# Kernel optimization log

Hardware: AMD Instinct MI355X
Metric: run time of the kernel (lower is better)

The kernel has to match this reference:

```python
import jax, jax.numpy as jnp
import numpy as np

B, C, H, W = 16, 256, 64, 64
K = 1024

def setup_inputs() -> dict:
    key = jax.random.key(0)
    k1, k2 = jax.random.split(key)
    x = jax.random.normal(k1, (B, C, H, W), dtype=jnp.float32)
    codebook = jax.random.normal(k2, (K, C), dtype=jnp.float32)
    return {"x": x, "codebook": codebook}


def reference(x, codebook):
    b, c, h, w = x.shape
    # (B, C, H, W) -> (B*H*W, C)
    xf = jnp.transpose(x, (0, 2, 3, 1)).reshape(-1, c)
    # Squared euclidean distances to codebook (argmin is the same as for cdist).
    x2 = jnp.sum(xf * xf, axis=-1, keepdims=True)          # (N, 1)
    c2 = jnp.sum(codebook * codebook, axis=-1)               # (K,)
    dist = x2 - 2.0 * jnp.einsum('nc,kc->nk', xf, codebook) + c2  # (N, K)
    idx = jnp.argmin(dist, axis=-1)                          # (N,)
    quant = codebook[idx]                                     # (N, C)
    commitment_loss = jnp.mean((jax.lax.stop_gradient(quant) - xf) ** 2)
    codebook_loss = jnp.mean((quant - jax.lax.stop_gradient(xf)) ** 2)
    # Straight-through estimator
    quant_out = xf + jax.lax.stop_gradient(quant - xf)
    quant_out = jnp.transpose(quant_out.reshape(b, h, w, c), (0, 3, 1, 2))
    indices = idx.reshape(b, h, w)
    return quant_out, codebook_loss, commitment_loss, indices
```

## Files before the change

kernel.cpp:

```cpp
#include <hip/hip_runtime.h>

constexpr int Bn = 16, Cd = 256, Hn = 64, Wn = 64, Kc = 1024;
constexpr int QUANT_ELEMS = Bn * Hn * Wn * Cd;
constexpr int LOSS_OFF = QUANT_ELEMS;
constexpr int IDX_OFF = QUANT_ELEMS + 2;

typedef _Float16 half8 __attribute__((ext_vector_type(8)));
typedef float f32x4 __attribute__((ext_vector_type(4)));

constexpr size_t WS_CBFH = 0;
constexpr size_t WS_CBFL = 512 * 1024;
constexpr size_t WS_C2   = 1024 * 1024;

constexpr float THR = 1e-4f;

__global__ __launch_bounds__(256) void prep(const float* __restrict__ cb,
                                            _Float16* __restrict__ cbFh,
                                            _Float16* __restrict__ cbFl,
                                            float* __restrict__ c2,
                                            float* __restrict__ out) {
    __shared__ float cbs[16][257];
    const int tid = threadIdx.x;
    const int k0 = blockIdx.x * 16;
    {
        const int c4 = (tid & 63) * 4;
        const int r0 = tid >> 6;
        #pragma unroll
        for (int it = 0; it < 4; ++it) {
            const int r = r0 + it * 4;
            const float4 v = *(const float4*)&cb[(size_t)(k0 + r) * Cd + c4];
            cbs[r][c4] = v.x; cbs[r][c4 + 1] = v.y; cbs[r][c4 + 2] = v.z; cbs[r][c4 + 3] = v.w;
        }
    }
    __syncthreads();
    {
        const int i = tid >> 4, part = tid & 15;
        float s = 0.f;
        #pragma unroll
        for (int c = part * 16; c < part * 16 + 16; ++c) { const float v = cbs[i][c]; s += v * v; }
        s += __shfl_xor(s, 1);
        s += __shfl_xor(s, 2);
        s += __shfl_xor(s, 4);
        s += __shfl_xor(s, 8);
        if (part == 0) c2[k0 + i] = s;
    }
    for (int t = tid; t < 512; t += 256) {
        const int kblk = t >> 6;
        const int l = t & 63;
        const int code_l = l & 15;
        const int cbase = kblk * 32 + (l >> 4) * 8;
        half8 hv, lv;
        #pragma unroll
        for (int j = 0; j < 8; ++j) {
            const float v = cbs[code_l][cbase + j];
            const _Float16 hh = (_Float16)v;
            hv[j] = hh;
            lv[j] = (_Float16)(v - (float)hh);
        }
        const size_t e = (size_t)(blockIdx.x * 8 + kblk) * 64 + l;
        *(half8*)(cbFh + e * 8) = hv;
        *(half8*)(cbFl + e * 8) = lv;
    }
    if (blockIdx.x == 0 && tid == 0) {
        out[LOSS_OFF] = 0.f; out[LOSS_OFF + 1] = 0.f;
    }
}

__global__ __launch_bounds__(512, 4) void vq_main(const float* __restrict__ x,
                                                  const _Float16* __restrict__ cbFh,
                                                  const _Float16* __restrict__ cbFl,
                                                  const float* __restrict__ c2,
                                                  const float* __restrict__ cb,
                                                  float* __restrict__ out) {
    __shared__ half8 Axh[2048];
    __shared__ half8 Axl[2048];
    __shared__ float q1ds[8][32];
    __shared__ int   q1is[8][32];
    __shared__ float q2ds[8][32];
    __shared__ int   q2is[8][32];
    __shared__ int   idx_s[64];
    __shared__ float red[8];
    __shared__ int   flg[64];
    __shared__ int   nflag;

    const int tid = threadIdx.x;
    const int lane = tid & 63;
    const int wv = tid >> 6;
    const int mth = wv & 1;
    const int ntq = wv >> 1;
    const int bh = blockIdx.x;
    const int b = bh >> 6, h = bh & 63;

    if (tid == 0) nflag = 0;

    {
        const int m = tid & 15;
        const int q = (tid >> 4) & 3;
        const int mtg = (tid >> 6) & 3;
        const int kh = tid >> 8;
        const int w = mtg * 16 + m;
        const float* xb = x + ((size_t)b * Cd * Hn + h) * Wn + w;
        #pragma unroll
        for (int kk = 0; kk < 4; ++kk) {
            const int kblk = kh * 4 + kk;
            half8 hv, lv;
            #pragma unroll
            for (int j = 0; j < 8; ++j) {
                const int c = kblk * 32 + q * 8 + j;
                const float v = xb[(size_t)c * (Hn * Wn)];
                const _Float16 hh = (_Float16)v;
                hv[j] = hh;
                lv[j] = (_Float16)(v - (float)hh);
            }
            const int e = (kblk * 4 + mtg) * 64 + (q * 16 + m);
            Axh[e] = hv;
            Axl[e] = lv;
        }
    }
    __syncthreads();

    float q1d[8], q2d[8];
    int   q1i[8], q2i[8];
    #pragma unroll
    for (int i = 0; i < 8; ++i) { q1d[i] = 3.4e38f; q2d[i] = 3.4e38f; q1i[i] = 0; q2i[i] = 0; }

    half8 nbh[2], nbl[2];
    #pragma unroll
    for (int nt = 0; nt < 2; ++nt) {
        const int ntile = ntq * 16 + nt;
        const size_t be = ((size_t)(ntile * 8) * 64 + lane) * 8;
        nbh[nt] = *(const half8*)(cbFh + be);
        nbl[nt] = *(const half8*)(cbFl + be);
    }

    #pragma unroll 1
    for (int grp = 0; grp < 8; ++grp) {
        f32x4 acc[2][2];
        acc[0][0] = (f32x4){0.f, 0.f, 0.f, 0.f};
        acc[0][1] = (f32x4){0.f, 0.f, 0.f, 0.f};
        acc[1][0] = (f32x4){0.f, 0.f, 0.f, 0.f};
        acc[1][1] = (f32x4){0.f, 0.f, 0.f, 0.f};

        #pragma unroll 2
        for (int kblk = 0; kblk < 8; ++kblk) {
            const half8 cbh0 = nbh[0], cbh1 = nbh[1];
            const half8 cbl0 = nbl[0], cbl1 = nbl[1];
            {
                const int nk = (kblk + 1) & 7;
                const int ng = (grp + ((kblk + 1) >> 3)) & 7;
                #pragma unroll
                for (int nt = 0; nt < 2; ++nt) {
                    const int ntile = ntq * 16 + ng * 2 + nt;
                    const size_t be = ((size_t)(ntile * 8 + nk) * 64 + lane) * 8;
                    nbh[nt] = *(const half8*)(cbFh + be);
                    nbl[nt] = *(const half8*)(cbFl + be);
                }
            }
            half8 ahf[2], alf[2];
            #pragma unroll
            for (int ml = 0; ml < 2; ++ml) {
                const int e = (kblk * 4 + mth * 2 + ml) * 64 + lane;
                ahf[ml] = Axh[e];
                alf[ml] = Axl[e];
            }
            #pragma unroll
            for (int ml = 0; ml < 2; ++ml) {
                acc[ml][0] = __builtin_amdgcn_mfma_f32_16x16x32_f16(ahf[ml], cbh0, acc[ml][0], 0, 0, 0);
                acc[ml][1] = __builtin_amdgcn_mfma_f32_16x16x32_f16(ahf[ml], cbh1, acc[ml][1], 0, 0, 0);
            }
            #pragma unroll
            for (int ml = 0; ml < 2; ++ml) {
                acc[ml][0] = __builtin_amdgcn_mfma_f32_16x16x32_f16(ahf[ml], cbl0, acc[ml][0], 0, 0, 0);
                acc[ml][1] = __builtin_amdgcn_mfma_f32_16x16x32_f16(ahf[ml], cbl1, acc[ml][1], 0, 0, 0);
            }
            #pragma unroll
            for (int ml = 0; ml < 2; ++ml) {
                acc[ml][0] = __builtin_amdgcn_mfma_f32_16x16x32_f16(alf[ml], cbh0, acc[ml][0], 0, 0, 0);
                acc[ml][1] = __builtin_amdgcn_mfma_f32_16x16x32_f16(alf[ml], cbh1, acc[ml][1], 0, 0, 0);
            }
        }

        #pragma unroll
        for (int nt = 0; nt < 2; ++nt) {
            const int code = (ntq * 16 + grp * 2 + nt) * 16 + (lane & 15);
            const float c2v = c2[code];
            #pragma unroll
            for (int ml = 0; ml < 2; ++ml) {
                #pragma unroll
                for (int reg = 0; reg < 4; ++reg) {
                    const float d = fmaf(-2.f, acc[ml][nt][reg], c2v);
                    const int qi = ml * 4 + reg;
                    const bool b1 = d < q1d[qi];
                    const bool b2 = d < q2d[qi];
                    q2d[qi] = b1 ? q1d[qi] : (b2 ? d : q2d[qi]);
                    q2i[qi] = b1 ? q1i[qi] : (b2 ? code : q2i[qi]);
                    q1d[qi] = b1 ? d : q1d[qi];
                    q1i[qi] = b1 ? code : q1i[qi];
                }
            }
        }
    }

    #pragma unroll
    for (int off = 1; off < 16; off <<= 1) {
        #pragma unroll
        for (int qi = 0; qi < 8; ++qi) {
            const float od1 = __shfl_xor(q1d[qi], off);
            const int   oi1 = __shfl_xor(q1i[qi], off);
            const float od2 = __shfl_xor(q2d[qi], off);
            const int   oi2 = __shfl_xor(q2i[qi], off);
            const bool ob = od1 < q1d[qi];
            const float ld = ob ? q1d[qi] : od1;
            const int   li = ob ? q1i[qi] : oi1;
            const bool o2 = od2 < q2d[qi];
            const float md = o2 ? od2 : q2d[qi];
            const int   mi = o2 ? oi2 : q2i[qi];
            const bool lb = ld < md;
            q2d[qi] = lb ? ld : md;
            q2i[qi] = lb ? li : mi;
            q1d[qi] = ob ? od1 : q1d[qi];
            q1i[qi] = ob ? oi1 : q1i[qi];
        }
    }
    if ((lane & 15) == 0) {
        #pragma unroll
        for (int qi = 0; qi < 8; ++qi) {
            const int ml = qi >> 2, reg = qi & 3;
            const int rl = ml * 16 + (lane >> 4) * 4 + reg;
            q1ds[wv][rl] = q1d[qi];
            q1is[wv][rl] = q1i[qi];
            q2ds[wv][rl] = q2d[qi];
            q2is[wv][rl] = q2i[qi];
        }
    }
    __syncthreads();
    if (tid < 64) {
        const int hh = tid >> 5, rl = tid & 31;
        float d1 = q1ds[hh][rl]; int i1 = q1is[hh][rl];
        float d2 = q2ds[hh][rl]; int i2 = q2is[hh][rl];
        #pragma unroll
        for (int v = 1; v < 4; ++v) {
            const int w2 = hh + 2 * v;
            const float od1 = q1ds[w2][rl]; const int oi1 = q1is[w2][rl];
            const float od2 = q2ds[w2][rl]; const int oi2 = q2is[w2][rl];
            const bool ob = od1 < d1;
            const float ld = ob ? d1 : od1;
            const int   li = ob ? i1 : oi1;
            const bool o2 = od2 < d2;
            const float md = o2 ? od2 : d2;
            const int   mi = o2 ? oi2 : i2;
            const bool lb = ld < md;
            d2 = lb ? ld : md;
            i2 = lb ? li : mi;
            d1 = ob ? od1 : d1;
            i1 = ob ? oi1 : i1;
        }
        idx_s[tid] = i1;
        if (d2 - d1 < THR) {
            const int pos = atomicAdd(&nflag, 1);
            flg[pos] = tid | (i2 << 6);
        }
    }
    __syncthreads();

    const int nf = nflag;
    for (int fi = 0; fi < nf; ++fi) {
        if (wv == 0) {
            const int pack = flg[fi];
            const int w = pack & 63;
            const int i2 = pack >> 6;
            const int i1 = idx_s[w];
            const int mt = w >> 4, m = w & 15;
            const _Float16* axh = (const _Float16*)Axh;
            const _Float16* axl = (const _Float16*)Axl;
            float s1 = 0.f, s2 = 0.f;
            #pragma unroll
            for (int cc = 0; cc < 4; ++cc) {
                const int c = lane * 4 + cc;
                const int kblk = c >> 5, q = (c >> 3) & 3, j = c & 7;
                const int e8 = ((kblk * 4 + mt) * 64 + q * 16 + m) * 8 + j;
                const float xv = (float)axh[e8] + (float)axl[e8];
                const float e1 = cb[(size_t)i1 * Cd + c] - xv;
                const float e2 = cb[(size_t)i2 * Cd + c] - xv;
                s1 = fmaf(e1, e1, s1);
                s2 = fmaf(e2, e2, s2);
            }
            #pragma unroll
            for (int off = 32; off >= 1; off >>= 1) {
                s1 += __shfl_xor(s1, off);
                s2 += __shfl_xor(s2, off);
            }
            if (lane == 0 && (s2 < s1 || (s2 == s1 && i2 < i1))) idx_s[w] = i2;
        }
    }
    __syncthreads();

    if (tid < 64) out[IDX_OFF + bh * 64 + tid] = (float)idx_s[tid];

    {
        const int w = tid & 63;
        const int kblk = wv;
        const int m = w & 15, mt = w >> 4;
        const int myidx = idx_s[w];
        const float4* cbrow = (const float4*)(cb + (size_t)myidx * Cd + kblk * 32);
        float lsum = 0.f;
        #pragma unroll
        for (int q = 0; q < 4; ++q) {
            const int e = (kblk * 4 + mt) * 64 + q * 16 + m;
            const half8 hv = Axh[e];
            const half8 lv = Axl[e];
            const float4 qa = cbrow[q * 2];
            const float4 qb = cbrow[q * 2 + 1];
            const float qv[8] = {qa.x, qa.y, qa.z, qa.w, qb.x, qb.y, qb.z, qb.w};
            const int cbase = kblk * 32 + q * 8;
            #pragma unroll
            for (int j = 0; j < 8; ++j) {
                const float xv = (float)hv[j] + (float)lv[j];
                const float dd = qv[j] - xv;
                lsum += dd * dd;
                out[(((size_t)b * Cd + cbase + j) * Hn + h) * Wn + w] = qv[j];
            }
        }
        #pragma unroll
        for (int off = 32; off >= 1; off >>= 1) lsum += __shfl_xor(lsum, off);
        if (lane == 0) red[wv] = lsum;
    }
    __syncthreads();
    if (tid == 0) {
        float s = 0.f;
        #pragma unroll
        for (int i = 0; i < 8; ++i) s += red[i];
        s *= (1.0f / 16777216.0f);
        atomicAdd(out + LOSS_OFF, s);
        atomicAdd(out + LOSS_OFF + 1, s);
    }
}

extern "C" void kernel_launch(void* const* d_in, const int* in_sizes, int n_in,
                              void* d_out, int out_size, void* d_ws, size_t ws_size,
                              hipStream_t stream) {
    const float* x  = (const float*)d_in[0];
    const float* cb = (const float*)d_in[1];
    float* out = (float*)d_out;
    char* ws = (char*)d_ws;
    _Float16* cbFh = (_Float16*)(ws + WS_CBFH);
    _Float16* cbFl = (_Float16*)(ws + WS_CBFL);
    float* c2      = (float*)(ws + WS_C2);

    prep<<<64, 256, 0, stream>>>(cb, cbFh, cbFl, c2, out);
    vq_main<<<Bn * Hn, 512, 0, stream>>>(x, cbFh, cbFl, c2, cb, out);
}
```

Measured before the change: 225.7 us.

## Double-buffer codebook prefetch, track top-2 distances only, full-scan flagged rows

Codebook fragments are now prefetched two k-blocks ahead into a two-slot register buffer, with the k loop fully unrolled, to hide global load latency. The top-2 tracking drops the second-best index and uses med3/min ops, which cuts VGPR use and select instructions. Rows whose best and second-best distances are close are now resolved by a block-wide fp32 scan over all 1024 codes instead of comparing two candidates. That scan is heavier per flagged row and adds barriers, but flags should be rare.

```diff
diff --git a/kernel.cpp b/kernel.cpp
--- a/kernel.cpp
+++ b/kernel.cpp
@@ -13,6 +13,14 @@
 constexpr size_t WS_C2   = 1024 * 1024;
 
 constexpr float THR = 1e-4f;
+
+static __device__ __forceinline__ float med3f(float a, float b, float c) {
+#if __has_builtin(__builtin_amdgcn_fmed3f)
+    return __builtin_amdgcn_fmed3f(a, b, c);
+#else
+    return fmaxf(fminf(a, b), fminf(fmaxf(a, b), c));
+#endif
+}
 
 __global__ __launch_bounds__(256) void prep(const float* __restrict__ cb,
                                             _Float16* __restrict__ cbFh,
@@ -77,11 +85,13 @@
     __shared__ float q1ds[8][32];
     __shared__ int   q1is[8][32];
     __shared__ float q2ds[8][32];
-    __shared__ int   q2is[8][32];
     __shared__ int   idx_s[64];
     __shared__ float red[8];
     __shared__ int   flg[64];
     __shared__ int   nflag;
+    __shared__ float scan_xs[256];
+    __shared__ float scan_d[8];
+    __shared__ int   scan_k[8];
 
     const int tid = threadIdx.x;
     const int lane = tid & 63;
@@ -120,17 +130,22 @@
     __syncthreads();
 
     float q1d[8], q2d[8];
-    int   q1i[8], q2i[8];
+    int   q1i[8];
     #pragma unroll
-    for (int i = 0; i < 8; ++i) { q1d[i] = 3.4e38f; q2d[i] = 3.4e38f; q1i[i] = 0; q2i[i] = 0; }
-
-    half8 nbh[2], nbl[2];
-    #pragma unroll
-    for (int nt = 0; nt < 2; ++nt) {
-        const int ntile = ntq * 16 + nt;
-        const size_t be = ((size_t)(ntile * 8) * 64 + lane) * 8;
-        nbh[nt] = *(const half8*)(cbFh + be);
-        nbl[nt] = *(const half8*)(cbFl + be);
+    for (int i = 0; i < 8; ++i) { q1d[i] = 3.4e38f; q2d[i] = 3.4e38f; q1i[i] = 0; }
+
+    half8 sbh[2][2], sbl[2][2];
+    {
+        #pragma unroll
+        for (int s = 0; s < 2; ++s) {
+            #pragma unroll
+            for (int nt = 0; nt < 2; ++nt) {
+                const int ntile = ntq * 16 + ((s >> 3) & 7) * 2 + nt;
+                const size_t be = ((size_t)(ntile * 8 + (s & 7)) * 64 + lane) * 8;
+                sbh[s][nt] = *(const half8*)(cbFh + be);
+                sbl[s][nt] = *(const half8*)(cbFl + be);
+            }
+        }
     }
 
     #pragma unroll 1
@@ -141,19 +156,20 @@
         acc[1][0] = (f32x4){0.f, 0.f, 0.f, 0.f};
         acc[1][1] = (f32x4){0.f, 0.f, 0.f, 0.f};
 
-        #pragma unroll 2
+        #pragma unroll
         for (int kblk = 0; kblk < 8; ++kblk) {
-            const half8 cbh0 = nbh[0], cbh1 = nbh[1];
-            const half8 cbl0 = nbl[0], cbl1 = nbl[1];
+            const int slot = kblk & 1;
+            const half8 cbh0 = sbh[slot][0], cbh1 = sbh[slot][1];
+            const half8 cbl0 = sbl[slot][0], cbl1 = sbl[slot][1];
             {
-                const int nk = (kblk + 1) & 7;
-                const int ng = (grp + ((kblk + 1) >> 3)) & 7;
+                const int sn = (grp * 8 + kblk + 2) & 63;
+                const int ng = sn >> 3, nk = sn & 7;
                 #pragma unroll
                 for (int nt = 0; nt < 2; ++nt) {
                     const int ntile = ntq * 16 + ng * 2 + nt;
                     const size_t be = ((size_t)(ntile * 8 + nk) * 64 + lane) * 8;
-                    nbh[nt] = *(const half8*)(cbFh + be);
-                    nbl[nt] = *(const half8*)(cbFl + be);
+                    sbh[slot][nt] = *(const half8*)(cbFh + be);
+                    sbl[slot][nt] = *(const half8*)(cbFl + be);
                 }
             }
             half8 ahf[2], alf[2];
@@ -190,12 +206,9 @@
                 for (int reg = 0; reg < 4; ++reg) {
                     const float d = fmaf(-2.f, acc[ml][nt][reg], c2v);
                     const int qi = ml * 4 + reg;
-                    const bool b1 = d < q1d[qi];
-                    const bool b2 = d < q2d[qi];
-                    q2d[qi] = b1 ? q1d[qi] : (b2 ? d : q2d[qi]);
-                    q2i[qi] = b1 ? q1i[qi] : (b2 ? code : q2i[qi]);
-                    q1d[qi] = b1 ? d : q1d[qi];
-                    q1i[qi] = b1 ? code : q1i[qi];
+                    q2d[qi] = med3f(q1d[qi], q2d[qi], d);
+                    q1i[qi] = (d < q1d[qi]) ? code : q1i[qi];
+                    q1d[qi] = fminf(q1d[qi], d);
                 }
             }
         }
@@ -208,18 +221,10 @@
             const float od1 = __shfl_xor(q1d[qi], off);
             const int   oi1 = __shfl_xor(q1i[qi], off);
             const float od2 = __shfl_xor(q2d[qi], off);
-            const int   oi2 = __shfl_xor(q2i[qi], off);
-            const bool ob = od1 < q1d[qi];
-            const float ld = ob ? q1d[qi] : od1;
-            const int   li = ob ? q1i[qi] : oi1;
-            const bool o2 = od2 < q2d[qi];
-            const float md = o2 ? od2 : q2d[qi];
-            const int   mi = o2 ? oi2 : q2i[qi];
-            const bool lb = ld < md;
-            q2d[qi] = lb ? ld : md;
-            q2i[qi] = lb ? li : mi;
-            q1d[qi] = ob ? od1 : q1d[qi];
-            q1i[qi] = ob ? oi1 : q1i[qi];
+            const float hi = fmaxf(q1d[qi], od1);
+            q2d[qi] = fminf(fminf(q2d[qi], od2), hi);
+            q1i[qi] = (od1 < q1d[qi]) ? oi1 : q1i[qi];
+            q1d[qi] = fminf(q1d[qi], od1);
         }
     }
     if ((lane & 15) == 0) {
@@ -230,70 +235,79 @@
             q1ds[wv][rl] = q1d[qi];
             q1is[wv][rl] = q1i[qi];
             q2ds[wv][rl] = q2d[qi];
-            q2is[wv][rl] = q2i[qi];
         }
     }
     __syncthreads();
     if (tid < 64) {
         const int hh = tid >> 5, rl = tid & 31;
-        float d1 = q1ds[hh][rl]; int i1 = q1is[hh][rl];
-        float d2 = q2ds[hh][rl]; int i2 = q2is[hh][rl];
+        float d1 = q1ds[hh][rl]; int i1 = q1is[hh][rl]; float d2 = q2ds[hh][rl];
         #pragma unroll
         for (int v = 1; v < 4; ++v) {
             const int w2 = hh + 2 * v;
             const float od1 = q1ds[w2][rl]; const int oi1 = q1is[w2][rl];
-            const float od2 = q2ds[w2][rl]; const int oi2 = q2is[w2][rl];
-            const bool ob = od1 < d1;
-            const float ld = ob ? d1 : od1;
-            const int   li = ob ? i1 : oi1;
-            const bool o2 = od2 < d2;
-            const float md = o2 ? od2 : d2;
-            const int   mi = o2 ? oi2 : i2;
-            const bool lb = ld < md;
-            d2 = lb ? ld : md;
-            i2 = lb ? li : mi;
-            d1 = ob ? od1 : d1;
-            i1 = ob ? oi1 : i1;
+            const float od2 = q2ds[w2][rl];
+            const float hi = fmaxf(d1, od1);
+            d2 = fminf(fminf(d2, od2), hi);
+            i1 = (od1 < d1) ? oi1 : i1;
+            d1 = fminf(d1, od1);
         }
         idx_s[tid] = i1;
         if (d2 - d1 < THR) {
             const int pos = atomicAdd(&nflag, 1);
-            flg[pos] = tid | (i2 << 6);
+            flg[pos] = tid;
         }
     }
     __syncthreads();
 
     const int nf = nflag;
     for (int fi = 0; fi < nf; ++fi) {
-        if (wv == 0) {
-            const int pack = flg[fi];
-            const int w = pack & 63;
-            const int i2 = pack >> 6;
-            const int i1 = idx_s[w];
-            const int mt = w >> 4, m = w & 15;
-            const _Float16* axh = (const _Float16*)Axh;
-            const _Float16* axl = (const _Float16*)Axl;
-            float s1 = 0.f, s2 = 0.f;
-            #pragma unroll
-            for (int cc = 0; cc < 4; ++cc) {
-                const int c = lane * 4 + cc;
-                const int kblk = c >> 5, q = (c >> 3) & 3, j = c & 7;
-                const int e8 = ((kblk * 4 + mt) * 64 + q * 16 + m) * 8 + j;
-                const float xv = (float)axh[e8] + (float)axl[e8];
-                const float e1 = cb[(size_t)i1 * Cd + c] - xv;
-                const float e2 = cb[(size_t)i2 * Cd + c] - xv;
-                s1 = fmaf(e1, e1, s1);
-                s2 = fmaf(e2, e2, s2);
-            }
-            #pragma unroll
-            for (int off = 32; off >= 1; off >>= 1) {
-                s1 += __shfl_xor(s1, off);
-                s2 += __shfl_xor(s2, off);
-            }
-            if (lane == 0 && (s2 < s1 || (s2 == s1 && i2 < i1))) idx_s[w] = i2;
-        }
-    }
-    __syncthreads();
+        const int wrow = flg[fi];
+        if (tid < 256) {
+            const int c = tid;
+            const int mt = wrow >> 4, m = wrow & 15;
+            const int e = ((c >> 5) * 4 + mt) * 64 + ((c >> 3) & 3) * 16 + m;
+            const int j = c & 7;
+            scan_xs[c] = (float)Axh[e][j] + (float)Axl[e][j];
+        }
+        __syncthreads();
+        float bd = 3.4e38f; int bk = 0;
+        #pragma unroll
+        for (int r = 0; r < 2; ++r) {
+            const int code = tid * 2 + r;
+            const float4* cr = (const float4*)(cb + (size_t)code * Cd);
+            const float4* xr = (const float4*)scan_xs;
+            float dot = 0.f;
+            #pragma unroll 8
+            for (int i = 0; i < 64; ++i) {
+                const float4 v = cr[i];
+                const float4 xv = xr[i];
+                dot = fmaf(v.x, xv.x, dot);
+                dot = fmaf(v.y, xv.y, dot);
+                dot = fmaf(v.z, xv.z, dot);
+                dot = fmaf(v.w, xv.w, dot);
+            }
+            const float d = c2[code] - 2.f * dot;
+            if (d < bd || (d == bd && code < bk)) { bd = d; bk = code; }
+        }
+        #pragma unroll
+        for (int off = 32; off >= 1; off >>= 1) {
+            const float od = __shfl_xor(bd, off);
+            const int   ok = __shfl_xor(bk, off);
+            if (od < bd || (od == bd && ok < bk)) { bd = od; bk = ok; }
+        }
+        if (lane == 0) { scan_d[wv] = bd; scan_k[wv] = bk; }
+        __syncthreads();
+        if (tid == 0) {
+            float fd = scan_d[0]; int fk = scan_k[0];
+            #pragma unroll
+            for (int v = 1; v < 8; ++v) {
+                const float od = scan_d[v]; const int ok = scan_k[v];
+                if (od < fd || (od == fd && ok < fk)) { fd = od; fk = ok; }
+            }
+            idx_s[wrow] = fk;
+        }
+        __syncthreads();
+    }
 
     if (tid < 64) out[IDX_OFF + bh * 64 + tid] = (float)idx_s[tid];
 
```

Measured after the change: 482.0 us. +113.5%, slower.
